# Performance work log

Measured on AMD Instinct MI355X. Metric: run time of the kernel, lower is better.

The kernel has to match this reference:

```python
import jax, jax.numpy as jnp
import numpy as np

N, E, IN, HID, OUT = 50000, 800000, 128, 96, 2


def setup_inputs() -> dict:
    key = jax.random.key(0)
    ks = jax.random.split(key, 10)
    x = jax.random.normal(ks[0], (N, IN), jnp.float32)
    edge_index = jax.random.randint(ks[1], (2, E), 0, N, dtype=jnp.int64)
    # PQVA mask: per-node, first output channel is a "known" quantity (masked out),
    # second is the prediction target -> ~mask selects exactly N elements.
    m = np.zeros((N, OUT), dtype=bool)
    m[:, 0] = True
    PQVA_mask = jnp.asarray(m)
    scaler_mean = 0.1 * jax.random.normal(ks[2], (IN,), jnp.float32)
    scaler_std = 0.5 + jax.random.uniform(ks[3], (IN,), jnp.float32)  # in [0.5, 1.5)
    W1 = jax.random.normal(ks[4], (IN, HID), jnp.float32) / np.sqrt(IN)
    W2 = jax.random.normal(ks[5], (HID, HID), jnp.float32) / np.sqrt(HID)
    W3 = jax.random.normal(ks[6], (HID, HID), jnp.float32) / np.sqrt(HID)
    Wout = jax.random.normal(ks[7], (HID, OUT), jnp.float32) / np.sqrt(HID)
    b1 = jnp.zeros((HID,), jnp.float32)
    b2 = jnp.zeros((HID,), jnp.float32)
    b3 = jnp.zeros((HID,), jnp.float32)
    bout = jnp.zeros((OUT,), jnp.float32)
    return {"x": x, "edge_index": edge_index, "PQVA_mask": PQVA_mask,
            "scaler_mean": scaler_mean, "scaler_std": scaler_std,
            "W1": W1, "b1": b1, "W2": W2, "b2": b2, "W3": W3, "b3": b3,
            "Wout": Wout, "bout": bout}


def reference(x, edge_index, PQVA_mask, scaler_mean, scaler_std,
              W1, b1, W2, b2, W3, b3, Wout, bout):
    n = x.shape[0]
    loop = jnp.arange(n, dtype=edge_index.dtype)
    src = jnp.concatenate([edge_index[0], loop])  # add self-loops (GCNConv default)
    dst = jnp.concatenate([edge_index[1], loop])
    deg = jax.ops.segment_sum(jnp.ones_like(dst, x.dtype), dst, num_segments=n)
    dinv = jax.lax.rsqrt(deg)  # deg >= 1 thanks to self-loops
    norm = (dinv[src] * dinv[dst])[:, None]  # [E+N, 1]

    def prop(h):  # D^-1/2 (A+I) D^-1/2 @ h  via gather-scale-scatter
        return jax.ops.segment_sum(h[src] * norm, dst, num_segments=n)

    h = (x - scaler_mean) / scaler_std          # standard scaler
    h = jax.nn.relu(prop(h @ W1) + b1)          # GCNConv 1 + ReLU
    h = jax.nn.relu(prop(h @ W2) + b2)          # GCNConv 2 + ReLU
    h = prop(h @ W3) + b3                       # GCNConv 3 (last, no act)
    out = h @ Wout + bout                       # final Linear -> [N, OUT]
    # masked reshape: ~mask has exactly one True per node -> [N]
    return out.reshape(-1)[~PQVA_mask.reshape(-1)]
```

## Files before the change

kernel.cpp:

```cpp
#include <hip/hip_runtime.h>
#include <hip/hip_fp16.h>

#define IN_F 128
#define HID_F 96
#define PB 512
#define STRIDE 6144
#define MAXB 8192

typedef _Float16 f16x8 __attribute__((ext_vector_type(8)));
typedef float f32x4 __attribute__((ext_vector_type(4)));

__device__ __forceinline__ void swizzle_one(const float* W, __half* Wsw, int idx) {
    int j  = idx & 7;
    int ln = (idx >> 3) & 63;
    int ct = idx >> 9;
    int t = ct % 6, c = ct / 6;
    int k   = c * 32 + (ln >> 4) * 8 + j;
    int col = t * 16 + (ln & 15);
    Wsw[idx] = (__half)W[k * 96 + col];
}

__global__ __launch_bounds__(256) void part_prep_kernel(
        const int* __restrict__ srcv, const int* __restrict__ dstv,
        int* __restrict__ bcur, int* __restrict__ ebuf, int E,
        const float* __restrict__ stdv, float* __restrict__ rstd,
        const float* __restrict__ W3, const float* __restrict__ Wout,
        const float* __restrict__ b3, const float* __restrict__ bout,
        float* __restrict__ wv, float* __restrict__ cconst,
        const float* __restrict__ W1, __half* __restrict__ Wsw1, int SW1,
        const float* __restrict__ W2, __half* __restrict__ Wsw2, int SW2) {
    int b = blockIdx.x, t = threadIdx.x;
    if (b >= PB) {
        int pb = b - PB;
        if (pb == 0) {
            if (t < IN_F) rstd[t] = 1.0f / stdv[t];
            if (t < HID_F) {
                float s = 0.f;
                for (int j = 0; j < HID_F; ++j) s += W3[t * HID_F + j] * Wout[j * 2 + 1];
                wv[t] = s;
            }
            if (t == 0) {
                float s = 0.f;
                for (int j = 0; j < HID_F; ++j) s += b3[j] * Wout[j * 2 + 1];
                cconst[0] = s + bout[1];
            }
        } else if (pb <= 48) {
            int idx = (pb - 1) * 256 + t;
            if (idx < SW1) swizzle_one(W1, Wsw1, idx);
        } else {
            int idx = (pb - 49) * 256 + t;
            if (idx < SW2) swizzle_one(W2, Wsw2, idx);
        }
        return;
    }
    __shared__ int h[256];
    __shared__ int cur[256];
    int chunk = (E + PB - 1) / PB;
    int s = b * chunk;
    int eend = min(s + chunk, E);
    h[t] = 0;
    __syncthreads();
    for (int e = s + t; e < eend; e += 256) atomicAdd(&h[dstv[e] >> 8], 1);
    __syncthreads();
    if (h[t]) cur[t] = t * STRIDE + atomicAdd(&bcur[t], h[t]);
    __syncthreads();
    for (int e = s + t; e < eend; e += 256) {
        int sv = srcv[e], d = dstv[e];
        int p = atomicAdd(&cur[d >> 8], 1);
        ebuf[p] = (sv << 8) | (d & 255);
    }
}

template<int MODE, int K, int SC>
__device__ __forceinline__ void gemm_body(
        int bid, int tid,
        const void* __restrict__ Ain, const __half* __restrict__ Wsw,
        const float* __restrict__ mean, const float* __restrict__ rstd,
        const float* __restrict__ dinv, __half* __restrict__ C, int n) {
    constexpr int NCH = K / 32;
    int lane = tid & 63;
    int wv_  = tid >> 6;
    int m = lane & 15, q = lane >> 4;
    int node0 = bid * 64 + wv_ * 16;
    int g = node0 + m;
    int gc = g < n ? g : n - 1;

    f32x4 acc[6];
#pragma unroll
    for (int t = 0; t < 6; ++t) acc[t] = (f32x4){0.f, 0.f, 0.f, 0.f};

#pragma unroll
    for (int c = 0; c < NCH; ++c) {
        f16x8 a;
        if (MODE == 0) {
            const float* ap = (const float*)Ain + (long)gc * K + c * 32 + q * 8;
            float4 v0 = *(const float4*)ap;
            float4 v1 = *(const float4*)(ap + 4);
            float4 m0 = *(const float4*)(mean + c * 32 + q * 8);
            float4 m1 = *(const float4*)(mean + c * 32 + q * 8 + 4);
            float4 r0 = *(const float4*)(rstd + c * 32 + q * 8);
            float4 r1 = *(const float4*)(rstd + c * 32 + q * 8 + 4);
            a[0] = (_Float16)((v0.x - m0.x) * r0.x);
            a[1] = (_Float16)((v0.y - m0.y) * r0.y);
            a[2] = (_Float16)((v0.z - m0.z) * r0.z);
            a[3] = (_Float16)((v0.w - m0.w) * r0.w);
            a[4] = (_Float16)((v1.x - m1.x) * r1.x);
            a[5] = (_Float16)((v1.y - m1.y) * r1.y);
            a[6] = (_Float16)((v1.z - m1.z) * r1.z);
            a[7] = (_Float16)((v1.w - m1.w) * r1.w);
        } else {
            a = *(const f16x8*)((const __half*)Ain + (long)gc * K + c * 32 + q * 8);
        }
#pragma unroll
        for (int t = 0; t < 6; ++t) {
            f16x8 b = *(const f16x8*)(Wsw + (size_t)(((c * 6) + t) * 64 + lane) * 8);
            acc[t] = __builtin_amdgcn_mfma_f32_16x16x32_f16(a, b, acc[t], 0, 0, 0);
        }
    }
    float dv[4];
#pragma unroll
    for (int r = 0; r < 4; ++r) {
        int gr = node0 + q * 4 + r;
        dv[r] = SC ? ((gr < n) ? dinv[gr] : 0.f) : 1.f;
    }
#pragma unroll
    for (int t = 0; t < 6; ++t)
#pragma unroll
        for (int r = 0; r < 4; ++r) {
            int gr = node0 + q * 4 + r;
            float o = SC ? acc[t][r] * dv[r] : acc[t][r];
            if (gr < n) C[(long)gr * 96 + t * 16 + m] = (__half)o;
        }
}

template<int MODE, int K, int SC>
__global__ __launch_bounds__(256) void gemm_mfma_kernel(
        const void* __restrict__ Ain, const __half* __restrict__ Wsw,
        const float* __restrict__ mean, const float* __restrict__ rstd,
        const float* __restrict__ dinv, __half* __restrict__ C, int n) {
    gemm_body<MODE, K, SC>(blockIdx.x, threadIdx.x, Ain, Wsw, mean, rstd, dinv, C, n);
}


__global__ __launch_bounds__(256) void csr_gemm1_kernel(
        const int* __restrict__ ebuf, const int* __restrict__ bcur,
        int* __restrict__ rowdeg, float* __restrict__ dinv,
        int* __restrict__ cols, int n, int nb,
        const float* __restrict__ x, const __half* __restrict__ Wsw1,
        const float* __restrict__ mean, const float* __restrict__ rstd,
        __half* __restrict__ C) {
    __shared__ int dg[256];
    __shared__ int tmp[256];
    __shared__ int cur[256];
    __shared__ int colst[MAXB];
    int t = threadIdx.x;
    if (blockIdx.x >= nb) {
        gemm_body<0, IN_F, 0>(blockIdx.x - nb, t, x, Wsw1, mean, rstd, nullptr, C, n);
        return;
    }
    int k = blockIdx.x;
    int seg = k * STRIDE;
    int cnt = min(bcur[k], STRIDE);
    dg[t] = 0;
    __syncthreads();
    for (int i = t; i < cnt; i += 256) atomicAdd(&dg[ebuf[seg + i] & 255], 1);
    __syncthreads();
    int v = dg[t];
    tmp[t] = v;
    __syncthreads();
#pragma unroll
    for (int off = 1; off < 256; off <<= 1) {
        int u = (t >= off) ? tmp[t - off] : 0;
        __syncthreads();
        tmp[t] += u;
        __syncthreads();
    }
    int excl = tmp[t] - v;
    int node = (k << 8) + t;
    if (node < n) {
        rowdeg[node] = ((seg + excl) << 9) | v;
        dinv[node] = rsqrtf((float)v + 1.0f);
    }
    cur[t] = excl;
    __syncthreads();
    for (int i = t; i < cnt; i += 256) {
        int p = ebuf[seg + i];
        int lp = atomicAdd(&cur[p & 255], 1);
        colst[lp] = ((unsigned)p) >> 8;
    }
    __syncthreads();
    for (int i = t; i < cnt; i += 256) cols[seg + i] = colst[i];
}


template<int DOT, int SCALE>
__global__ __launch_bounds__(256) void prop4_kernel(
        const __half* __restrict__ hin, const int* __restrict__ rowdeg,
        const int* __restrict__ cols,
        const float* __restrict__ dinv, const float* __restrict__ bias,
        const float* __restrict__ wvv, __half* __restrict__ hout,
        float* __restrict__ zs, int n) {
    int wid  = (blockIdx.x * blockDim.x + threadIdx.x) >> 6;
    int lane = threadIdx.x & 63;
    int g = lane >> 4;
    int l = lane & 15;
    int node = wid * 4 + g;
    bool nvalid = node < n;
    int nodec = nvalid ? node : n - 1;
    int rd = rowdeg[nodec];
    int e0 = ((unsigned)rd) >> 9;
    int deg = rd & 511;
    float di = dinv[nodec];
    const f16x8* hp = (const f16x8*)hin;
    int lc = l < 12 ? l : 0;

    f16x8 vself = hp[(long)nodec * 12 + lc];
    float sself = SCALE ? di : 1.f;
    float acc[8];
#pragma unroll
    for (int j = 0; j < 8; ++j) acc[j] = sself * (float)vself[j];

    for (int eb = 0; eb < deg; eb += 16) {
        int rem = deg - eb;
        if (rem > 16) rem = 16;
        int idx = eb + l;
        int colv = __builtin_nontemporal_load(&cols[e0 + (idx < deg ? idx : 0)]);
        float dvl = SCALE ? dinv[colv] : 1.f;
        for (int k0 = 0; k0 < rem; k0 += 8) {
            int c[8];
            float s[8];
#pragma unroll
            for (int kk = 0; kk < 8; ++kk) {
                int p = k0 + kk;
                int srcl = (g << 4) + p;
                int cc = __shfl(colv, srcl, 64);
                float dd = __shfl(dvl, srcl, 64);
                bool is = p < rem;
                c[kk] = is ? cc : nodec;
                s[kk] = is ? (SCALE ? dd : 1.f) : 0.f;
            }
            f16x8 v[8];
#pragma unroll
            for (int kk = 0; kk < 8; ++kk) v[kk] = hp[(long)c[kk] * 12 + lc];
#pragma unroll
            for (int kk = 0; kk < 8; ++kk)
#pragma unroll
                for (int j = 0; j < 8; ++j)
                    acc[j] = fmaf((float)v[kk][j], s[kk], acc[j]);
        }
    }

    if (DOT == 0) {
        if (nvalid && l < 12) {
            float4 b0 = *(const float4*)(bias + l * 8);
            float4 b1 = *(const float4*)(bias + l * 8 + 4);
            f16x8 o;
            o[0] = (_Float16)fmaxf(di * acc[0] + b0.x, 0.f);
            o[1] = (_Float16)fmaxf(di * acc[1] + b0.y, 0.f);
            o[2] = (_Float16)fmaxf(di * acc[2] + b0.z, 0.f);
            o[3] = (_Float16)fmaxf(di * acc[3] + b0.w, 0.f);
            o[4] = (_Float16)fmaxf(di * acc[4] + b1.x, 0.f);
            o[5] = (_Float16)fmaxf(di * acc[5] + b1.y, 0.f);
            o[6] = (_Float16)fmaxf(di * acc[6] + b1.z, 0.f);
            o[7] = (_Float16)fmaxf(di * acc[7] + b1.w, 0.f);
            __builtin_nontemporal_store(o, (f16x8*)(hout + (long)node * 96 + l * 8));
        }
    } else {
        float v = 0.f;
        if (l < 12) {
            float4 b0 = *(const float4*)(bias + l * 8);
            float4 b1 = *(const float4*)(bias + l * 8 + 4);
            float4 w0 = *(const float4*)(wvv + l * 8);
            float4 w1 = *(const float4*)(wvv + l * 8 + 4);
            v  = fmaxf(di * acc[0] + b0.x, 0.f) * w0.x;
            v += fmaxf(di * acc[1] + b0.y, 0.f) * w0.y;
            v += fmaxf(di * acc[2] + b0.z, 0.f) * w0.z;
            v += fmaxf(di * acc[3] + b0.w, 0.f) * w0.w;
            v += fmaxf(di * acc[4] + b1.x, 0.f) * w1.x;
            v += fmaxf(di * acc[5] + b1.y, 0.f) * w1.y;
            v += fmaxf(di * acc[6] + b1.z, 0.f) * w1.z;
            v += fmaxf(di * acc[7] + b1.w, 0.f) * w1.w;
        }
        v += __shfl_xor(v, 1, 64);
        v += __shfl_xor(v, 2, 64);
        v += __shfl_xor(v, 4, 64);
        v += __shfl_xor(v, 8, 64);
        if (nvalid && l == 0) __builtin_nontemporal_store(di * v, &zs[node]);
    }
}


__global__ __launch_bounds__(256) void prop_scalar_kernel(
        const float* __restrict__ zs, const int* __restrict__ rowdeg,
        const int* __restrict__ cols,
        const float* __restrict__ dinv, const float* __restrict__ cconst,
        float* __restrict__ out, int n) {
    int i = blockIdx.x * blockDim.x + threadIdx.x;
    if (i >= n) return;
    int rd = rowdeg[i];
    int e0 = ((unsigned)rd) >> 9;
    int e1 = e0 + (rd & 511);
    float s = 0.f;
    int e = e0;
    for (; e + 8 <= e1; e += 8) {
        int c[8];
#pragma unroll
        for (int k = 0; k < 8; ++k) c[k] = __builtin_nontemporal_load(&cols[e + k]);
        float z[8];
#pragma unroll
        for (int k = 0; k < 8; ++k) z[k] = zs[c[k]];
#pragma unroll
        for (int k = 0; k < 8; ++k) s += z[k];
    }
    for (; e < e1; ++e) s += zs[__builtin_nontemporal_load(&cols[e])];
    out[i] = dinv[i] * (s + zs[i]) + cconst[0];
}

extern "C" void kernel_launch(void* const* d_in, const int* in_sizes, int n_in,
                              void* d_out, int out_size, void* d_ws, size_t ws_size,
                              hipStream_t stream) {
    const float* x    = (const float*)d_in[0];
    const int*   eidx = (const int*)d_in[1];
    const float* mean = (const float*)d_in[3];
    const float* stdv = (const float*)d_in[4];
    const float* W1   = (const float*)d_in[5];
    const float* b1   = (const float*)d_in[6];
    const float* W2   = (const float*)d_in[7];
    const float* b2   = (const float*)d_in[8];
    const float* W3   = (const float*)d_in[9];
    const float* b3   = (const float*)d_in[10];
    const float* Wout = (const float*)d_in[11];
    const float* bout = (const float*)d_in[12];
    float* out = (float*)d_out;

    const int n = in_sizes[0] / IN_F;
    const int E = in_sizes[1] / 2;
    const int* srcv = eidx;
    const int* dstv = eidx + E;
    const int NB = (n + 255) >> 8;

    char* ws = (char*)d_ws;
    size_t off = 0;
    auto alloc = [&](size_t bytes) -> void* {
        void* p = ws + off;
        off = (off + bytes + 255) & ~(size_t)255;
        return p;
    };
    const int SW1 = 4 * 6 * 64 * 8;
    const int SW2 = 3 * 6 * 64 * 8;
    int*    rowdeg = (int*)alloc((size_t)n * 4);
    float*  dinv   = (float*)alloc((size_t)n * 4);
    int*    cols   = (int*)alloc((size_t)256 * STRIDE * 4);
    int*    ebuf   = (int*)alloc((size_t)256 * STRIDE * 4);
    int*    bcur   = (int*)alloc(256 * 4);
    float*  rstd   = (float*)alloc(IN_F * 4);
    float*  wvv    = (float*)alloc(HID_F * 4);
    float*  cconst = (float*)alloc(4);
    float*  zbuf   = (float*)alloc((size_t)n * 4);
    __half* Wsw1   = (__half*)alloc((size_t)SW1 * 2);
    __half* Wsw2   = (__half*)alloc((size_t)SW2 * 2);
    __half* bufA   = (__half*)alloc((size_t)n * HID_F * 2);
    __half* bufB   = (__half*)alloc((size_t)n * HID_F * 2);

    (void)hipMemsetAsync(bcur, 0, 256 * 4, stream);

    part_prep_kernel<<<PB + 85, 256, 0, stream>>>(
        srcv, dstv, bcur, ebuf, E,
        stdv, rstd, W3, Wout, b3, bout, wvv, cconst,
        W1, Wsw1, SW1, W2, Wsw2, SW2);

    int gemm_grid = (n + 63) / 64;
    int wpg = (n + 3) / 4;
    int prop_grid = (int)(((long)wpg * 64 + 255) / 256);

    csr_gemm1_kernel<<<NB + gemm_grid, 256, 0, stream>>>(
        ebuf, bcur, rowdeg, dinv, cols, n, NB, x, Wsw1, mean, rstd, bufA);

    prop4_kernel<0, 1><<<prop_grid, 256, 0, stream>>>(bufA, rowdeg, cols, dinv, b1,
                                                      nullptr, bufB, nullptr, n);
    gemm_mfma_kernel<1, HID_F, 1><<<gemm_grid, 256, 0, stream>>>(
        bufB, Wsw2, nullptr, nullptr, dinv, bufA, n);
    prop4_kernel<1, 0><<<prop_grid, 256, 0, stream>>>(bufA, rowdeg, cols, dinv, b2,
                                                      wvv, nullptr, zbuf, n);
    prop_scalar_kernel<<<(n + 255) / 256, 256, 0, stream>>>(zbuf, rowdeg, cols, dinv,
                                                            cconst, out, n);
}
```

Measured before the change: 196.2 us.

## Sort nodes by degree within each block to balance propagation wavefronts

Adds a per-256-node-block counting sort by in-degree in the CSR build kernel, producing a permutation array. The propagation kernels and the final scalar propagation then process nodes in that permuted order, so nodes handled by the same wavefront have similar degrees and idle lanes from uneven edge loops are reduced. The cost is an extra scan and histogram in the build kernel, one extra indirection load per node, and less contiguous access to node rows and outputs.

```diff
diff --git a/kernel.cpp b/kernel.cpp
--- a/kernel.cpp
+++ b/kernel.cpp
@@ -145,7 +145,7 @@
 __global__ __launch_bounds__(256) void csr_gemm1_kernel(
         const int* __restrict__ ebuf, const int* __restrict__ bcur,
         int* __restrict__ rowdeg, float* __restrict__ dinv,
-        int* __restrict__ cols, int n, int nb,
+        int* __restrict__ cols, int* __restrict__ perm, int n, int nb,
         const float* __restrict__ x, const __half* __restrict__ Wsw1,
         const float* __restrict__ mean, const float* __restrict__ rstd,
         __half* __restrict__ C) {
@@ -190,13 +190,33 @@
     }
     __syncthreads();
     for (int i = t; i < cnt; i += 256) cols[seg + i] = colst[i];
-}
-
+
+    __syncthreads();
+    dg[t] = 0;
+    __syncthreads();
+    int key = (node < n) ? min(v, 254) : 255;
+    atomicAdd(&dg[key], 1);
+    __syncthreads();
+    int hv = dg[t];
+    tmp[t] = hv;
+    __syncthreads();
+#pragma unroll
+    for (int off = 1; off < 256; off <<= 1) {
+        int u = (t >= off) ? tmp[t - off] : 0;
+        __syncthreads();
+        tmp[t] += u;
+        __syncthreads();
+    }
+    cur[t] = tmp[t] - hv;
+    __syncthreads();
+    int rank = atomicAdd(&cur[key], 1);
+    perm[(k << 8) + rank] = node;
+}
 
 template<int DOT, int SCALE>
 __global__ __launch_bounds__(256) void prop4_kernel(
         const __half* __restrict__ hin, const int* __restrict__ rowdeg,
-        const int* __restrict__ cols,
+        const int* __restrict__ cols, const int* __restrict__ perm,
         const float* __restrict__ dinv, const float* __restrict__ bias,
         const float* __restrict__ wvv, __half* __restrict__ hout,
         float* __restrict__ zs, int n) {
@@ -204,7 +224,7 @@
     int lane = threadIdx.x & 63;
     int g = lane >> 4;
     int l = lane & 15;
-    int node = wid * 4 + g;
+    int node = perm[wid * 4 + g];
     bool nvalid = node < n;
     int nodec = nvalid ? node : n - 1;
     int rd = rowdeg[nodec];
@@ -289,14 +309,14 @@
     }
 }
 
-
 __global__ __launch_bounds__(256) void prop_scalar_kernel(
         const float* __restrict__ zs, const int* __restrict__ rowdeg,
-        const int* __restrict__ cols,
+        const int* __restrict__ cols, const int* __restrict__ perm,
         const float* __restrict__ dinv, const float* __restrict__ cconst,
         float* __restrict__ out, int n) {
-    int i = blockIdx.x * blockDim.x + threadIdx.x;
-    if (i >= n) return;
+    int slot = blockIdx.x * blockDim.x + threadIdx.x;
+    if (slot >= n) return;
+    int i = perm[slot];
     int rd = rowdeg[i];
     int e0 = ((unsigned)rd) >> 9;
     int e1 = e0 + (rd & 511);
@@ -353,6 +373,7 @@
     int*    cols   = (int*)alloc((size_t)256 * STRIDE * 4);
     int*    ebuf   = (int*)alloc((size_t)256 * STRIDE * 4);
     int*    bcur   = (int*)alloc(256 * 4);
+    int*    perm   = (int*)alloc((size_t)NB * 256 * 4);
     float*  rstd   = (float*)alloc(IN_F * 4);
     float*  wvv    = (float*)alloc(HID_F * 4);
     float*  cconst = (float*)alloc(4);
@@ -374,14 +395,14 @@
     int prop_grid = (int)(((long)wpg * 64 + 255) / 256);
 
     csr_gemm1_kernel<<<NB + gemm_grid, 256, 0, stream>>>(
-        ebuf, bcur, rowdeg, dinv, cols, n, NB, x, Wsw1, mean, rstd, bufA);
-
-    prop4_kernel<0, 1><<<prop_grid, 256, 0, stream>>>(bufA, rowdeg, cols, dinv, b1,
+        ebuf, bcur, rowdeg, dinv, cols, perm, n, NB, x, Wsw1, mean, rstd, bufA);
+
+    prop4_kernel<0, 1><<<prop_grid, 256, 0, stream>>>(bufA, rowdeg, cols, perm, dinv, b1,
                                                       nullptr, bufB, nullptr, n);
     gemm_mfma_kernel<1, HID_F, 1><<<gemm_grid, 256, 0, stream>>>(
         bufB, Wsw2, nullptr, nullptr, dinv, bufA, n);
-    prop4_kernel<1, 0><<<prop_grid, 256, 0, stream>>>(bufA, rowdeg, cols, dinv, b2,
+    prop4_kernel<1, 0><<<prop_grid, 256, 0, stream>>>(bufA, rowdeg, cols, perm, dinv, b2,
                                                       wvv, nullptr, zbuf, n);
-    prop_scalar_kernel<<<(n + 255) / 256, 256, 0, stream>>>(zbuf, rowdeg, cols, dinv,
-                                                            cconst, out, n);
-}
+    prop_scalar_kernel<<<(n + 255) / 256, 256, 0, stream>>>(zbuf, rowdeg, cols, perm,
+                                                            dinv, cconst, out, n);
+}
```

Result: slower. 212.0 us (+8.1%).
